# Kernel tuning notes

Measured on AMD Instinct MI355X. Metric: run time of the kernel, lower is better.

The kernel has to match this reference:

```python
import jax, jax.numpy as jnp
import numpy as np

EPS = 1e-9


def _pairwise_sqdist(x1, x2):
    # x1: (B,n,3), x2: (B,m,3) -> (B,n,m) squared euclidean distances
    s1 = jnp.sum(x1 * x1, axis=-1)
    s2 = jnp.sum(x2 * x2, axis=-1)
    cross = jnp.einsum('bnd,bmd->bnm', x1, x2)
    return jnp.maximum(s1[:, :, None] + s2[:, None, :] - 2.0 * cross, 0.0)


def _approxmatch(x1, x2):
    # Faithful port of the approxmatch CUDA kernel (Fan et al. EMD approx).
    B, n, _ = x1.shape
    m = x2.shape[1]
    if n >= m:
        multiL, multiR = 1.0, float(n // m)   # integer division as in CUDA
    else:
        multiL, multiR = float(m // n), 1.0
    dist = _pairwise_sqdist(x1, x2)  # (B,n,m)
    # j = 7 .. -1 -> level = -4^j ; j = -2 -> level = 0  (10 sweeps total)
    levels = jnp.concatenate([
        -(4.0 ** jnp.arange(7, -2, -1, dtype=jnp.float32)),
        jnp.zeros((1,), jnp.float32)])
    match0 = jnp.zeros((B, n, m), jnp.float32)
    remainL0 = jnp.full((B, n), multiL, jnp.float32)
    remainR0 = jnp.full((B, m), multiR, jnp.float32)

    def body(carry, level):
        match, remainL, remainR = carry
        e = jnp.exp(level * dist)                              # (B,n,m)
        suml = EPS + jnp.einsum('bnm,bm->bn', e, remainR)
        ratioL = remainL / suml                                # (B,n)
        sumr = remainR * jnp.einsum('bnm,bn->bm', e, ratioL)   # (B,m)
        consumption = jnp.minimum(remainR / (sumr + EPS), 1.0)
        ratioR = consumption * remainR                         # (B,m)
        remainR = jnp.maximum(0.0, remainR - sumr)
        w = e * ratioL[:, :, None] * ratioR[:, None, :]        # flow k->l
        match = match + w
        remainL = jnp.maximum(0.0, remainL - jnp.sum(w, axis=-1))
        return (match, remainL, remainR), None

    (match, _, _), _ = jax.lax.scan(body, (match0, remainL0, remainR0), levels)
    return match, dist


def setup_inputs() -> dict:
    key = jax.random.key(0)
    k1, k2 = jax.random.split(key)
    B, N = 4, 4096
    xyz1 = jax.random.normal(k1, (B, 3, N), dtype=jnp.float32)
    xyz2 = jax.random.normal(k2, (B, 3, N), dtype=jnp.float32)
    return {"xyz1": xyz1, "xyz2": xyz2}


def reference(xyz1, xyz2):
    # transpose=True: BCN -> BNC
    x1 = jnp.transpose(xyz1, (0, 2, 1))
    x2 = jnp.transpose(xyz2, (0, 2, 1))
    match, dist = _approxmatch(x1, x2)
    d = jnp.sqrt(jnp.maximum(dist, 1e-20))
    cost = jnp.sum(match * d, axis=(1, 2))            # (B,)
    emd = cost / min(x1.shape[1], x2.shape[1])
    return jnp.mean(emd)                               # reduce_mean=True
```

## Files before the change

### kernel.cpp

```cpp
#include <hip/hip_runtime.h>


#define NPTS 4096
#define BATCH 4
#define EMD_EPS 1e-9f
#define TILE 1024
#define RPW 4
#define THREADS 256
#define RPB 16
#define NBLK (NPTS / RPB)
#define NBLK_TOTAL (NBLK * BATCH)

#define GRP_SHIFT 4
#define GRP_SIZE (1 << GRP_SHIFT)
#define NGRP (NBLK_TOTAL / GRP_SIZE)
#define BAR_STRIDE 4352
#define NB_BAR 24

#define CULL_FULL -160.0f
#define CULL_PART -40.0f

typedef float v2f __attribute__((ext_vector_type(2)));

struct Params {
    const float* xyz1;
    const float* xyz2;
    float* remainL;
    float* cost_part;
    float* S_L;
    float* out;
    unsigned* bar;
    float* ratioL[10];
    float* ratioR[9];
    float* remainR[9];
    float ls2[10];
};

struct Smem {
    float4 sA[TILE / 2];
    float4 sB[TILE / 2];
    float2 sC[TILE / 2];
    float  s_cost[THREADS / 64];
};

__device__ __forceinline__ float aload(const float* p_) {
    return __hip_atomic_load((float*)p_, __ATOMIC_RELAXED, __HIP_MEMORY_SCOPE_AGENT);
}
__device__ __forceinline__ void astore(float* p_, float v) {
    __hip_atomic_store(p_, v, __ATOMIC_RELAXED, __HIP_MEMORY_SCOPE_AGENT);
}
__device__ __forceinline__ unsigned au_add(unsigned* p_, unsigned v) {
    return __hip_atomic_fetch_add(p_, v, __ATOMIC_RELAXED, __HIP_MEMORY_SCOPE_AGENT);
}
__device__ __forceinline__ unsigned au_load(const unsigned* p_) {
    return __hip_atomic_load((unsigned*)p_, __ATOMIC_RELAXED, __HIP_MEMORY_SCOPE_AGENT);
}
__device__ __forceinline__ void au_store(unsigned* p_, unsigned v) {
    __hip_atomic_store(p_, v, __ATOMIC_RELAXED, __HIP_MEMORY_SCOPE_AGENT);
}

__device__ __forceinline__ void gsync(unsigned* barbase, int idx) {
    __syncthreads();
    if (threadIdx.x == 0) {
        unsigned* B = barbase + idx * BAR_STRIDE;
        const int bid = blockIdx.y * NBLK + blockIdx.x;
        const int grp = bid >> GRP_SHIFT;
        unsigned* gc   = B + grp * 32;
        unsigned* root = B + NGRP * 32;
        unsigned* gr   = B + NGRP * 32 + 32 + grp * 32;
        unsigned old = au_add(gc, 1u);
        if (old == GRP_SIZE - 1u) {
            unsigned r = au_add(root, 1u) + 1u;
            while (r < (unsigned)NGRP) {
                __builtin_amdgcn_s_sleep(4);
                r = au_load(root);
            }
            au_store(gr, 1u);
        } else {
            while (au_load(gr) == 0u)
                __builtin_amdgcn_s_sleep(4);
        }
        asm volatile("" ::: "memory");
    }
    __syncthreads();
}

__device__ __forceinline__ float fexp2(float x) {
#if __has_builtin(__builtin_amdgcn_exp2f)
    return __builtin_amdgcn_exp2f(x);
#else
    return exp2f(x);
#endif
}
__device__ __forceinline__ float fsqrt(float x) {
#if __has_builtin(__builtin_amdgcn_sqrtf)
    return __builtin_amdgcn_sqrtf(x);
#else
    return __sqrtf(x);
#endif
}

__device__ __forceinline__ float wave_reduce(float v) {
    v += __shfl_xor(v, 32);
    v += __shfl_xor(v, 16);
    v += __shfl_xor(v, 8);
    v += __shfl_xor(v, 4);
    v += __shfl_xor(v, 2);
    v += __shfl_xor(v, 1);
    return v;
}

__device__ __forceinline__ void phase_ratioL0(Smem& sm, const Params& p, float ls2,
                                              float* __restrict__ rLout) {
    const int b = blockIdx.y;
    const int tid = threadIdx.x;
    const int wave = tid >> 6;
    const int lane = tid & 63;
    const int row0 = blockIdx.x * RPB + wave * RPW;

    const float* x1 = p.xyz1 + b * 3 * NPTS;
    const float* x2 = p.xyz2 + b * 3 * NPTS;
    const float2* x2x = (const float2*)(x2);
    const float2* x2y = (const float2*)(x2 + NPTS);
    const float2* x2z = (const float2*)(x2 + 2 * NPTS);

    float px[RPW], py[RPW], pz[RPW];
    v2f acc[RPW];
#pragma unroll
    for (int r = 0; r < RPW; ++r) {
        px[r] = x1[row0 + r];
        py[r] = x1[NPTS + row0 + r];
        pz[r] = x1[2 * NPTS + row0 + r];
        acc[r] = (v2f)(0.0f);
    }
    for (int c0 = 0; c0 < NPTS; c0 += TILE) {
        __syncthreads();
        for (int i = tid; i < TILE / 2; i += THREADS) {
            int e = c0 / 2 + i;
            float2 xx = x2x[e], yy = x2y[e];
            sm.sA[i] = make_float4(xx.x, xx.y, yy.x, yy.y);
            sm.sC[i] = x2z[e];
        }
        __syncthreads();
#pragma unroll 2
        for (int j = 0; j < TILE / 128; ++j) {
            float4 a = sm.sA[lane + 64 * j];
            float2 z = sm.sC[lane + 64 * j];
            v2f ax = {a.x, a.y}, ay = {a.z, a.w}, az = {z.x, z.y};
#pragma unroll
            for (int r = 0; r < RPW; ++r) {
                v2f dx = px[r] - ax, dy = py[r] - ay, dz = pz[r] - az;
                v2f d = dx * dx + dy * dy + dz * dz;
                v2f sd = ls2 * d;
                if (!__all(fmaxf(sd.x, sd.y) < CULL_FULL)) {
                    v2f e2 = {fexp2(sd.x), fexp2(sd.y)};
                    acc[r] += e2;
                }
            }
        }
    }
#pragma unroll
    for (int r = 0; r < RPW; ++r) {
        float s = wave_reduce(acc[r].x + acc[r].y);
        if (lane == 0) {
            int idx = b * NPTS + row0 + r;
            astore(&rLout[idx], 1.0f / (EMD_EPS + s));
            p.remainL[idx] = 1.0f;
        }
    }
}

template <bool CULL>
__device__ __forceinline__ void phase_ratioR(Smem& sm, const Params& p, float ls2,
                                             const float* __restrict__ rL,
                                             const float* __restrict__ rRprev,
                                             float* __restrict__ rRout,
                                             float* __restrict__ remROut) {
    const int b = blockIdx.y;
    const int tid = threadIdx.x;
    const int wave = tid >> 6;
    const int lane = tid & 63;
    const int col0 = blockIdx.x * RPB + wave * RPW;

    const float* x1 = p.xyz1 + b * 3 * NPTS;
    const float* x2 = p.xyz2 + b * 3 * NPTS;
    const float2* x1x = (const float2*)(x1);
    const float2* x1y = (const float2*)(x1 + NPTS);
    const float2* x1z = (const float2*)(x1 + 2 * NPTS);
    const float2* wLv = (const float2*)(rL + b * NPTS);

    float px[RPW], py[RPW], pz[RPW];
    v2f acc[RPW];
#pragma unroll
    for (int r = 0; r < RPW; ++r) {
        px[r] = x2[col0 + r];
        py[r] = x2[NPTS + col0 + r];
        pz[r] = x2[2 * NPTS + col0 + r];
        acc[r] = (v2f)(0.0f);
    }
    for (int c0 = 0; c0 < NPTS; c0 += TILE) {
        __syncthreads();
        for (int i = tid; i < TILE / 2; i += THREADS) {
            int e = c0 / 2 + i;
            float2 xx = x1x[e], yy = x1y[e], zz = x1z[e], ww = wLv[e];
            sm.sA[i] = make_float4(xx.x, xx.y, yy.x, yy.y);
            sm.sB[i] = make_float4(zz.x, zz.y, ww.x, ww.y);
        }
        __syncthreads();
#pragma unroll 2
        for (int j = 0; j < TILE / 128; ++j) {
            float4 a = sm.sA[lane + 64 * j];
            float4 bq = sm.sB[lane + 64 * j];
            v2f ax = {a.x, a.y}, ay = {a.z, a.w};
            v2f az = {bq.x, bq.y}, aw = {bq.z, bq.w};
#pragma unroll
            for (int r = 0; r < RPW; ++r) {
                v2f dx = px[r] - ax, dy = py[r] - ay, dz = pz[r] - az;
                v2f d = dx * dx + dy * dy + dz * dz;
                v2f sd = ls2 * d;
                bool live = true;
                if (CULL) live = !__all(fmaxf(sd.x, sd.y) < CULL_FULL);
                if (live) {
                    v2f e2 = {fexp2(sd.x), fexp2(sd.y)};
                    acc[r] += e2 * aw;
                }
            }
        }
    }
#pragma unroll
    for (int r = 0; r < RPW; ++r) {
        float s = wave_reduce(acc[r].x + acc[r].y);
        if (lane == 0) {
            int idx = b * NPTS + col0 + r;
            float rv = rRprev ? rRprev[idx] : 1.0f;
            float sumr = rv * s;
            float cons = fminf(rv / (sumr + EMD_EPS), 1.0f);
            astore(&rRout[idx], cons * rv);
            astore(&remROut[idx], fmaxf(0.0f, rv - sumr));
        }
    }
}

template <bool SQ, bool CULL>
__device__ __forceinline__ void phase_cost(Smem& sm, const Params& p,
                                           float ls2, float ls2n,
                                           const float* __restrict__ rR,
                                           const float* __restrict__ w2,
                                           const float* __restrict__ rLin,
                                           float* __restrict__ rLout,
                                           int initCost) {
    const int b = blockIdx.y;
    const int tid = threadIdx.x;
    const int wave = tid >> 6;
    const int lane = tid & 63;
    const int row0 = blockIdx.x * RPB + wave * RPW;

    const float* x1 = p.xyz1 + b * 3 * NPTS;
    const float* x2 = p.xyz2 + b * 3 * NPTS;
    const float2* x2x = (const float2*)(x2);
    const float2* x2y = (const float2*)(x2 + NPTS);
    const float2* x2z = (const float2*)(x2 + 2 * NPTS);
    const float2* wRv = (const float2*)(rR + b * NPTS);
    const float2* w2v = (const float2*)(w2 + b * NPTS);

    float px[RPW], py[RPW], pz[RPW];
    v2f acc_a[RPW], acc_c[RPW], acc_s[RPW];
#pragma unroll
    for (int r = 0; r < RPW; ++r) {
        px[r] = x1[row0 + r];
        py[r] = x1[NPTS + row0 + r];
        pz[r] = x1[2 * NPTS + row0 + r];
        acc_a[r] = (v2f)(0.0f);
        acc_c[r] = (v2f)(0.0f);
        acc_s[r] = (v2f)(0.0f);
    }
    for (int c0 = 0; c0 < NPTS; c0 += TILE) {
        __syncthreads();
        for (int i = tid; i < TILE / 2; i += THREADS) {
            int e = c0 / 2 + i;
            float2 xx = x2x[e], yy = x2y[e], zz = x2z[e];
            float2 wr = wRv[e];
            float2 cw = w2v[e];
            sm.sA[i] = make_float4(xx.x, xx.y, yy.x, yy.y);
            sm.sB[i] = make_float4(zz.x, zz.y, wr.x, wr.y);
            sm.sC[i] = cw;
        }
        __syncthreads();
#pragma unroll 2
        for (int j = 0; j < TILE / 128; ++j) {
            float4 a = sm.sA[lane + 64 * j];
            float4 bq = sm.sB[lane + 64 * j];
            float2 c = sm.sC[lane + 64 * j];
            v2f ax = {a.x, a.y}, ay = {a.z, a.w};
            v2f az = {bq.x, bq.y}, wr = {bq.z, bq.w};
            v2f cw = {c.x, c.y};
#pragma unroll
            for (int r = 0; r < RPW; ++r) {
                v2f dx = px[r] - ax, dy = py[r] - ay, dz = pz[r] - az;
                v2f d = dx * dx + dy * dy + dz * dz;
                if (SQ) {
                    v2f sd = ls2n * d;
                    bool fullskip = false, partskip = false;
                    if (CULL) {
                        float mx = fmaxf(sd.x, sd.y);
                        fullskip = __all(mx < CULL_FULL);
                        partskip = __all(mx < CULL_PART);
                    }
                    if (!fullskip) {
                        v2f e2 = {fexp2(sd.x), fexp2(sd.y)};
                        acc_s[r] += e2 * cw;
                        if (!partskip) {
                            v2f e4 = e2 * e2;
                            v2f er = (e4 * e4) * wr;
                            acc_a[r] += er;
                            v2f sq = {fsqrt(d.x), fsqrt(d.y)};
                            acc_c[r] += er * sq;
                        }
                    }
                } else {
                    v2f sd = ls2 * d;
                    v2f e1 = {fexp2(sd.x), fexp2(sd.y)};
                    v2f er = e1 * wr;
                    acc_s[r] += cw;
                    acc_a[r] += er;
                    v2f sq = {fsqrt(d.x), fsqrt(d.y)};
                    acc_c[r] += er * sq;
                }
            }
        }
    }
    float wcost = 0.0f;
#pragma unroll
    for (int r = 0; r < RPW; ++r) {
        float sa = wave_reduce(acc_a[r].x + acc_a[r].y);
        float sc = wave_reduce(acc_c[r].x + acc_c[r].y);
        float ss = wave_reduce(acc_s[r].x + acc_s[r].y);
        if (lane == 0) {
            int idx = b * NPTS + row0 + r;
            float rl = rLin[idx];
            float rem = fmaxf(0.0f, p.remainL[idx] - rl * sa);
            p.remainL[idx] = rem;
            astore(&rLout[idx], rem / (EMD_EPS + ss));
            wcost = fmaf(rl, sc, wcost);
        }
    }
    if (lane == 0) sm.s_cost[wave] = wcost;
    __syncthreads();
    if (tid == 0) {
        float t = sm.s_cost[0] + sm.s_cost[1] + sm.s_cost[2] + sm.s_cost[3];
        int ci = b * NBLK + blockIdx.x;
        astore(&p.cost_part[ci], initCost ? t : aload(&p.cost_part[ci]) + t);
    }
}

__device__ __forceinline__ void phase_sum_ratioL(Smem& sm, const Params& p,
                                                 const float* __restrict__ rL) {
    if (blockIdx.x != 0) return;
    const int b = blockIdx.y;
    const int tid = threadIdx.x;
    float s = 0.0f;
    for (int i = tid; i < NPTS; i += 256) s += rL[b * NPTS + i];
    s = wave_reduce(s);
    if ((tid & 63) == 0) sm.s_cost[tid >> 6] = s;
    __syncthreads();
    if (tid == 0)
        astore(&p.S_L[b], sm.s_cost[0] + sm.s_cost[1] + sm.s_cost[2] + sm.s_cost[3]);
}

__device__ __forceinline__ void phase_cost_l0(Smem& sm, const Params& p,
                                              const float* __restrict__ w2,
                                              const float* __restrict__ rL) {
    const int b = blockIdx.y;
    const int tid = threadIdx.x;
    const int wave = tid >> 6;
    const int lane = tid & 63;
    const int row0 = blockIdx.x * RPB + wave * RPW;
    const float sL = aload(&p.S_L[b]);

    const float* x1 = p.xyz1 + b * 3 * NPTS;
    const float* x2 = p.xyz2 + b * 3 * NPTS;
    const float2* x2x = (const float2*)(x2);
    const float2* x2y = (const float2*)(x2 + NPTS);
    const float2* x2z = (const float2*)(x2 + 2 * NPTS);
    const float2* wRv = (const float2*)(w2 + b * NPTS);

    float px[RPW], py[RPW], pz[RPW];
    v2f acc_c[RPW];
#pragma unroll
    for (int r = 0; r < RPW; ++r) {
        px[r] = x1[row0 + r];
        py[r] = x1[NPTS + row0 + r];
        pz[r] = x1[2 * NPTS + row0 + r];
        acc_c[r] = (v2f)(0.0f);
    }
    for (int c0 = 0; c0 < NPTS; c0 += TILE) {
        __syncthreads();
        for (int i = tid; i < TILE / 2; i += THREADS) {
            int e = c0 / 2 + i;
            float2 xx = x2x[e], yy = x2y[e], zz = x2z[e], rv = wRv[e];
            float wr0 = fminf(rv.x / (rv.x * sL + EMD_EPS), 1.0f) * rv.x;
            float wr1 = fminf(rv.y / (rv.y * sL + EMD_EPS), 1.0f) * rv.y;
            sm.sA[i] = make_float4(xx.x, xx.y, yy.x, yy.y);
            sm.sB[i] = make_float4(zz.x, zz.y, wr0, wr1);
        }
        __syncthreads();
#pragma unroll 2
        for (int j = 0; j < TILE / 128; ++j) {
            float4 a = sm.sA[lane + 64 * j];
            float4 bq = sm.sB[lane + 64 * j];
            v2f ax = {a.x, a.y}, ay = {a.z, a.w};
            v2f az = {bq.x, bq.y}, wr = {bq.z, bq.w};
#pragma unroll
            for (int r = 0; r < RPW; ++r) {
                v2f dx = px[r] - ax, dy = py[r] - ay, dz = pz[r] - az;
                v2f d = dx * dx + dy * dy + dz * dz;
                v2f sq = {fsqrt(d.x), fsqrt(d.y)};
                acc_c[r] += wr * sq;
            }
        }
    }
    float wcost = 0.0f;
#pragma unroll
    for (int r = 0; r < RPW; ++r) {
        float sc = wave_reduce(acc_c[r].x + acc_c[r].y);
        if (lane == 0)
            wcost = fmaf(rL[b * NPTS + row0 + r], sc, wcost);
    }
    if (lane == 0) sm.s_cost[wave] = wcost;
    __syncthreads();
    if (tid == 0) {
        float t = sm.s_cost[0] + sm.s_cost[1] + sm.s_cost[2] + sm.s_cost[3];
        int ci = b * NBLK + blockIdx.x;
        astore(&p.cost_part[ci], aload(&p.cost_part[ci]) + t);
    }
}

__device__ __forceinline__ void phase_final(Smem& sm, const Params& p) {
    if (blockIdx.x != 0 || blockIdx.y != 0) return;
    const int tid = threadIdx.x;
    float s = 0.0f;
    for (int i = tid; i < BATCH * NBLK; i += 256) s += aload(&p.cost_part[i]);
    s = wave_reduce(s);
    if ((tid & 63) == 0) sm.s_cost[tid >> 6] = s;
    __syncthreads();
    if (tid == 0)
        p.out[0] = (sm.s_cost[0] + sm.s_cost[1] + sm.s_cost[2] + sm.s_cost[3]) /
                   ((float)NPTS * (float)BATCH);
}

__global__ __launch_bounds__(THREADS, 4) void k_emd_all(Params p) {
    __shared__ Smem sm;
    int bi = 0;
    phase_ratioL0(sm, p, p.ls2[0], p.ratioL[0]);
    gsync(p.bar, bi++);
    for (int t = 0; t < 9; ++t) {
        const float* rRprev = (t == 0) ? nullptr : p.remainR[t - 1];
        if (t < 4)
            phase_ratioR<true>(sm, p, p.ls2[t], p.ratioL[t], rRprev,
                               p.ratioR[t], p.remainR[t]);
        else
            phase_ratioR<false>(sm, p, p.ls2[t], p.ratioL[t], rRprev,
                                p.ratioR[t], p.remainR[t]);
        gsync(p.bar, bi++);
        if (t < 4)
            phase_cost<true, true>(sm, p, p.ls2[t], p.ls2[t + 1], p.ratioR[t],
                                   p.remainR[t], p.ratioL[t], p.ratioL[t + 1], t == 0);
        else if (t < 8)
            phase_cost<true, false>(sm, p, p.ls2[t], p.ls2[t + 1], p.ratioR[t],
                                    p.remainR[t], p.ratioL[t], p.ratioL[t + 1], 0);
        else
            phase_cost<false, false>(sm, p, p.ls2[8], 0.0f, p.ratioR[8],
                                     p.remainR[8], p.ratioL[8], p.ratioL[9], 0);
        gsync(p.bar, bi++);
    }
    phase_sum_ratioL(sm, p, p.ratioL[9]);
    gsync(p.bar, bi++);
    phase_cost_l0(sm, p, p.remainR[8], p.ratioL[9]);
    gsync(p.bar, bi++);
    phase_final(sm, p);
}

__global__ void k_zero(unsigned* bar) {
    const int n = NB_BAR * BAR_STRIDE;
    for (int i = blockIdx.x * 256 + threadIdx.x; i < n; i += gridDim.x * 256)
        __hip_atomic_store(&bar[i], 0u, __ATOMIC_RELAXED, __HIP_MEMORY_SCOPE_AGENT);
}

__global__ __launch_bounds__(THREADS, 4) void kw_ratioL0(Params p) {
    __shared__ Smem sm;
    phase_ratioL0(sm, p, p.ls2[0], p.ratioL[0]);
}
__global__ __launch_bounds__(THREADS, 4) void kw_ratioR(Params p, int t) {
    __shared__ Smem sm;
    const float* rRprev = (t == 0) ? nullptr : p.remainR[t - 1];
    if (t < 4) phase_ratioR<true>(sm, p, p.ls2[t], p.ratioL[t], rRprev,
                                  p.ratioR[t], p.remainR[t]);
    else       phase_ratioR<false>(sm, p, p.ls2[t], p.ratioL[t], rRprev,
                                   p.ratioR[t], p.remainR[t]);
}
__global__ __launch_bounds__(THREADS, 4) void kw_cost(Params p, int t) {
    __shared__ Smem sm;
    if (t < 4)
        phase_cost<true, true>(sm, p, p.ls2[t], p.ls2[t + 1], p.ratioR[t],
                               p.remainR[t], p.ratioL[t], p.ratioL[t + 1], t == 0);
    else if (t < 8)
        phase_cost<true, false>(sm, p, p.ls2[t], p.ls2[t + 1], p.ratioR[t],
                                p.remainR[t], p.ratioL[t], p.ratioL[t + 1], 0);
    else
        phase_cost<false, false>(sm, p, p.ls2[8], 0.0f, p.ratioR[8],
                                 p.remainR[8], p.ratioL[8], p.ratioL[9], 0);
}
__global__ __launch_bounds__(THREADS, 4) void kw_sum(Params p) {
    __shared__ Smem sm;
    phase_sum_ratioL(sm, p, p.ratioL[9]);
}
__global__ __launch_bounds__(THREADS, 4) void kw_cost_l0(Params p) {
    __shared__ Smem sm;
    phase_cost_l0(sm, p, p.remainR[8], p.ratioL[9]);
}
__global__ __launch_bounds__(THREADS, 4) void kw_final(Params p) {
    __shared__ Smem sm;
    phase_final(sm, p);
}

extern "C" void kernel_launch(void* const* d_in, const int* in_sizes, int n_in,
                              void* d_out, int out_size, void* d_ws, size_t ws_size,
                              hipStream_t stream) {
    Params p;
    p.xyz1 = (const float*)d_in[0];
    p.xyz2 = (const float*)d_in[1];
    const int BN = BATCH * NPTS;
    const int BUF = BN + 1024;
    float* ws = (float*)d_ws;
    p.remainL   = ws;
    p.cost_part = ws + BN;
    p.S_L       = p.cost_part + 2048;
    p.bar       = (unsigned*)(p.S_L + 256);
    float* vbase = (float*)(p.bar + NB_BAR * BAR_STRIDE) + 256;
    for (int t = 0; t < 10; ++t) p.ratioL[t]  = vbase + t * BUF;
    for (int t = 0; t < 9; ++t)  p.ratioR[t]  = vbase + (10 + t) * BUF;
    for (int t = 0; t < 9; ++t)  p.remainR[t] = vbase + (19 + t) * BUF;
    p.out = (float*)d_out;

    static const double levels[10] = {
        -16384.0, -4096.0, -1024.0, -256.0, -64.0,
        -16.0, -4.0, -1.0, -0.25, 0.0};
    for (int t = 0; t < 10; ++t)
        p.ls2[t] = (float)(levels[t] * 1.4426950408889634);

    dim3 grid(NBLK, BATCH), blk(THREADS);

    static int coop_ok = -1;
    if (coop_ok < 0) {
        int v = 0;
        hipDeviceGetAttribute(&v, hipDeviceAttributeCooperativeLaunch, 0);
        coop_ok = v;
    }

    hipError_t err = hipErrorUnknown;
    if (coop_ok) {
        k_zero<<<64, 256, 0, stream>>>(p.bar);
        void* args[] = {(void*)&p};
        err = hipLaunchCooperativeKernel((void*)k_emd_all, grid, blk, args, 0, stream);
    }
    if (err != hipSuccess) {
        kw_ratioL0<<<grid, blk, 0, stream>>>(p);
        for (int t = 0; t < 9; ++t) {
            kw_ratioR<<<grid, blk, 0, stream>>>(p, t);
            kw_cost<<<grid, blk, 0, stream>>>(p, t);
        }
        kw_sum<<<dim3(1, BATCH), blk, 0, stream>>>(p);
        kw_cost_l0<<<grid, blk, 0, stream>>>(p);
        kw_final<<<dim3(1, 1), blk, 0, stream>>>(p);
    }
}
```

Measured before the change: 655.7 us.

## Stage full point clouds in LDS once and use 1024-thread blocks

```diff
diff --git a/kernel.cpp b/kernel.cpp
--- a/kernel.cpp
+++ b/kernel.cpp
@@ -4,12 +4,13 @@
 #define NPTS 4096
 #define BATCH 4
 #define EMD_EPS 1e-9f
-#define TILE 1024
 #define RPW 4
-#define THREADS 256
-#define RPB 16
+#define THREADS 1024
+#define NWAVE (THREADS / 64)
+#define RPB (NWAVE * RPW)
 #define NBLK (NPTS / RPB)
 #define NBLK_TOTAL (NBLK * BATCH)
+#define NJ (NPTS / 128)
 
 #define GRP_SHIFT 4
 #define GRP_SIZE (1 << GRP_SHIFT)
@@ -37,10 +38,15 @@
 };
 
 struct Smem {
-    float4 sA[TILE / 2];
-    float4 sB[TILE / 2];
-    float2 sC[TILE / 2];
-    float  s_cost[THREADS / 64];
+    alignas(16) float x1x[NPTS];
+    alignas(16) float x1y[NPTS];
+    alignas(16) float x1z[NPTS];
+    alignas(16) float x2x[NPTS];
+    alignas(16) float x2y[NPTS];
+    alignas(16) float x2z[NPTS];
+    alignas(16) float sW[NPTS];
+    alignas(16) float sV[NPTS];
+    float s_cost[NWAVE];
 };
 
 __device__ __forceinline__ float aload(const float* p_) {
@@ -110,6 +116,30 @@
     return v;
 }
 
+__device__ __forceinline__ void stage_xyz(Smem& sm, const Params& p) {
+    const int b = blockIdx.y;
+    const int i = threadIdx.x;
+    const float4* g1 = (const float4*)(p.xyz1 + b * 3 * NPTS);
+    const float4* g2 = (const float4*)(p.xyz2 + b * 3 * NPTS);
+    ((float4*)sm.x1x)[i] = g1[i];
+    ((float4*)sm.x1y)[i] = g1[NPTS / 4 + i];
+    ((float4*)sm.x1z)[i] = g1[2 * (NPTS / 4) + i];
+    ((float4*)sm.x2x)[i] = g2[i];
+    ((float4*)sm.x2y)[i] = g2[NPTS / 4 + i];
+    ((float4*)sm.x2z)[i] = g2[2 * (NPTS / 4) + i];
+    __syncthreads();
+}
+
+__device__ __forceinline__ void stage_w1(Smem& sm, const float* gw) {
+    ((float4*)sm.sW)[threadIdx.x] = ((const float4*)gw)[threadIdx.x];
+    __syncthreads();
+}
+__device__ __forceinline__ void stage_w2(Smem& sm, const float* gw, const float* gv) {
+    ((float4*)sm.sW)[threadIdx.x] = ((const float4*)gw)[threadIdx.x];
+    ((float4*)sm.sV)[threadIdx.x] = ((const float4*)gv)[threadIdx.x];
+    __syncthreads();
+}
+
 __device__ __forceinline__ void phase_ratioL0(Smem& sm, const Params& p, float ls2,
                                               float* __restrict__ rLout) {
     const int b = blockIdx.y;
@@ -118,44 +148,30 @@
     const int lane = tid & 63;
     const int row0 = blockIdx.x * RPB + wave * RPW;
 
-    const float* x1 = p.xyz1 + b * 3 * NPTS;
-    const float* x2 = p.xyz2 + b * 3 * NPTS;
-    const float2* x2x = (const float2*)(x2);
-    const float2* x2y = (const float2*)(x2 + NPTS);
-    const float2* x2z = (const float2*)(x2 + 2 * NPTS);
-
     float px[RPW], py[RPW], pz[RPW];
     v2f acc[RPW];
 #pragma unroll
     for (int r = 0; r < RPW; ++r) {
-        px[r] = x1[row0 + r];
-        py[r] = x1[NPTS + row0 + r];
-        pz[r] = x1[2 * NPTS + row0 + r];
+        px[r] = sm.x1x[row0 + r];
+        py[r] = sm.x1y[row0 + r];
+        pz[r] = sm.x1z[row0 + r];
         acc[r] = (v2f)(0.0f);
     }
-    for (int c0 = 0; c0 < NPTS; c0 += TILE) {
-        __syncthreads();
-        for (int i = tid; i < TILE / 2; i += THREADS) {
-            int e = c0 / 2 + i;
-            float2 xx = x2x[e], yy = x2y[e];
-            sm.sA[i] = make_float4(xx.x, xx.y, yy.x, yy.y);
-            sm.sC[i] = x2z[e];
-        }
-        __syncthreads();
+    const v2f* vx = (const v2f*)sm.x2x;
+    const v2f* vy = (const v2f*)sm.x2y;
+    const v2f* vz = (const v2f*)sm.x2z;
 #pragma unroll 2
-        for (int j = 0; j < TILE / 128; ++j) {
-            float4 a = sm.sA[lane + 64 * j];
-            float2 z = sm.sC[lane + 64 * j];
-            v2f ax = {a.x, a.y}, ay = {a.z, a.w}, az = {z.x, z.y};
-#pragma unroll
-            for (int r = 0; r < RPW; ++r) {
-                v2f dx = px[r] - ax, dy = py[r] - ay, dz = pz[r] - az;
-                v2f d = dx * dx + dy * dy + dz * dz;
-                v2f sd = ls2 * d;
-                if (!__all(fmaxf(sd.x, sd.y) < CULL_FULL)) {
-                    v2f e2 = {fexp2(sd.x), fexp2(sd.y)};
-                    acc[r] += e2;
-                }
+    for (int j = 0; j < NJ; ++j) {
+        int cp = lane + 64 * j;
+        v2f ax = vx[cp], ay = vy[cp], az = vz[cp];
+#pragma unroll
+        for (int r = 0; r < RPW; ++r) {
+            v2f dx = px[r] - ax, dy = py[r] - ay, dz = pz[r] - az;
+            v2f d = dx * dx + dy * dy + dz * dz;
+            v2f sd = ls2 * d;
+            if (!__all(fmaxf(sd.x, sd.y) < CULL_FULL)) {
+                v2f e2 = {fexp2(sd.x), fexp2(sd.y)};
+                acc[r] += e2;
             }
         }
     }
@@ -182,48 +198,35 @@
     const int lane = tid & 63;
     const int col0 = blockIdx.x * RPB + wave * RPW;
 
-    const float* x1 = p.xyz1 + b * 3 * NPTS;
-    const float* x2 = p.xyz2 + b * 3 * NPTS;
-    const float2* x1x = (const float2*)(x1);
-    const float2* x1y = (const float2*)(x1 + NPTS);
-    const float2* x1z = (const float2*)(x1 + 2 * NPTS);
-    const float2* wLv = (const float2*)(rL + b * NPTS);
+    stage_w1(sm, rL + b * NPTS);
 
     float px[RPW], py[RPW], pz[RPW];
     v2f acc[RPW];
 #pragma unroll
     for (int r = 0; r < RPW; ++r) {
-        px[r] = x2[col0 + r];
-        py[r] = x2[NPTS + col0 + r];
-        pz[r] = x2[2 * NPTS + col0 + r];
+        px[r] = sm.x2x[col0 + r];
+        py[r] = sm.x2y[col0 + r];
+        pz[r] = sm.x2z[col0 + r];
         acc[r] = (v2f)(0.0f);
     }
-    for (int c0 = 0; c0 < NPTS; c0 += TILE) {
-        __syncthreads();
-        for (int i = tid; i < TILE / 2; i += THREADS) {
-            int e = c0 / 2 + i;
-            float2 xx = x1x[e], yy = x1y[e], zz = x1z[e], ww = wLv[e];
-            sm.sA[i] = make_float4(xx.x, xx.y, yy.x, yy.y);
-            sm.sB[i] = make_float4(zz.x, zz.y, ww.x, ww.y);
-        }
-        __syncthreads();
+    const v2f* vx = (const v2f*)sm.x1x;
+    const v2f* vy = (const v2f*)sm.x1y;
+    const v2f* vz = (const v2f*)sm.x1z;
+    const v2f* vw = (const v2f*)sm.sW;
 #pragma unroll 2
-        for (int j = 0; j < TILE / 128; ++j) {
-            float4 a = sm.sA[lane + 64 * j];
-            float4 bq = sm.sB[lane + 64 * j];
-            v2f ax = {a.x, a.y}, ay = {a.z, a.w};
-            v2f az = {bq.x, bq.y}, aw = {bq.z, bq.w};
-#pragma unroll
-            for (int r = 0; r < RPW; ++r) {
-                v2f dx = px[r] - ax, dy = py[r] - ay, dz = pz[r] - az;
-                v2f d = dx * dx + dy * dy + dz * dz;
-                v2f sd = ls2 * d;
-                bool live = true;
-                if (CULL) live = !__all(fmaxf(sd.x, sd.y) < CULL_FULL);
-                if (live) {
-                    v2f e2 = {fexp2(sd.x), fexp2(sd.y)};
-                    acc[r] += e2 * aw;
-                }
+    for (int j = 0; j < NJ; ++j) {
+        int cp = lane + 64 * j;
+        v2f ax = vx[cp], ay = vy[cp], az = vz[cp], aw = vw[cp];
+#pragma unroll
+        for (int r = 0; r < RPW; ++r) {
+            v2f dx = px[r] - ax, dy = py[r] - ay, dz = pz[r] - az;
+            v2f d = dx * dx + dy * dy + dz * dz;
+            v2f sd = ls2 * d;
+            bool live = true;
+            if (CULL) live = !__all(fmaxf(sd.x, sd.y) < CULL_FULL);
+            if (live) {
+                v2f e2 = {fexp2(sd.x), fexp2(sd.y)};
+                acc[r] += e2 * aw;
             }
         }
     }
@@ -255,77 +258,60 @@
     const int lane = tid & 63;
     const int row0 = blockIdx.x * RPB + wave * RPW;
 
-    const float* x1 = p.xyz1 + b * 3 * NPTS;
-    const float* x2 = p.xyz2 + b * 3 * NPTS;
-    const float2* x2x = (const float2*)(x2);
-    const float2* x2y = (const float2*)(x2 + NPTS);
-    const float2* x2z = (const float2*)(x2 + 2 * NPTS);
-    const float2* wRv = (const float2*)(rR + b * NPTS);
-    const float2* w2v = (const float2*)(w2 + b * NPTS);
+    stage_w2(sm, rR + b * NPTS, w2 + b * NPTS);
 
     float px[RPW], py[RPW], pz[RPW];
     v2f acc_a[RPW], acc_c[RPW], acc_s[RPW];
 #pragma unroll
     for (int r = 0; r < RPW; ++r) {
-        px[r] = x1[row0 + r];
-        py[r] = x1[NPTS + row0 + r];
-        pz[r] = x1[2 * NPTS + row0 + r];
+        px[r] = sm.x1x[row0 + r];
+        py[r] = sm.x1y[row0 + r];
+        pz[r] = sm.x1z[row0 + r];
         acc_a[r] = (v2f)(0.0f);
         acc_c[r] = (v2f)(0.0f);
         acc_s[r] = (v2f)(0.0f);
     }
-    for (int c0 = 0; c0 < NPTS; c0 += TILE) {
-        __syncthreads();
-        for (int i = tid; i < TILE / 2; i += THREADS) {
-            int e = c0 / 2 + i;
-            float2 xx = x2x[e], yy = x2y[e], zz = x2z[e];
-            float2 wr = wRv[e];
-            float2 cw = w2v[e];
-            sm.sA[i] = make_float4(xx.x, xx.y, yy.x, yy.y);
-            sm.sB[i] = make_float4(zz.x, zz.y, wr.x, wr.y);
-            sm.sC[i] = cw;
-        }
-        __syncthreads();
+    const v2f* vx = (const v2f*)sm.x2x;
+    const v2f* vy = (const v2f*)sm.x2y;
+    const v2f* vz = (const v2f*)sm.x2z;
+    const v2f* vw = (const v2f*)sm.sW;
+    const v2f* vv = (const v2f*)sm.sV;
 #pragma unroll 2
-        for (int j = 0; j < TILE / 128; ++j) {
-            float4 a = sm.sA[lane + 64 * j];
-            float4 bq = sm.sB[lane + 64 * j];
-            float2 c = sm.sC[lane + 64 * j];
-            v2f ax = {a.x, a.y}, ay = {a.z, a.w};
-            v2f az = {bq.x, bq.y}, wr = {bq.z, bq.w};
-            v2f cw = {c.x, c.y};
-#pragma unroll
-            for (int r = 0; r < RPW; ++r) {
-                v2f dx = px[r] - ax, dy = py[r] - ay, dz = pz[r] - az;
-                v2f d = dx * dx + dy * dy + dz * dz;
-                if (SQ) {
-                    v2f sd = ls2n * d;
-                    bool fullskip = false, partskip = false;
-                    if (CULL) {
-                        float mx = fmaxf(sd.x, sd.y);
-                        fullskip = __all(mx < CULL_FULL);
-                        partskip = __all(mx < CULL_PART);
+    for (int j = 0; j < NJ; ++j) {
+        int cp = lane + 64 * j;
+        v2f ax = vx[cp], ay = vy[cp], az = vz[cp];
+        v2f wr = vw[cp], cw = vv[cp];
+#pragma unroll
+        for (int r = 0; r < RPW; ++r) {
+            v2f dx = px[r] - ax, dy = py[r] - ay, dz = pz[r] - az;
+            v2f d = dx * dx + dy * dy + dz * dz;
+            if (SQ) {
+                v2f sd = ls2n * d;
+                bool fullskip = false, partskip = false;
+                if (CULL) {
+                    float mx = fmaxf(sd.x, sd.y);
+                    fullskip = __all(mx < CULL_FULL);
+                    partskip = __all(mx < CULL_PART);
+                }
+                if (!fullskip) {
+                    v2f e2 = {fexp2(sd.x), fexp2(sd.y)};
+                    acc_s[r] += e2 * cw;
+                    if (!partskip) {
+                        v2f e4 = e2 * e2;
+                        v2f er = (e4 * e4) * wr;
+                        acc_a[r] += er;
+                        v2f sq = {fsqrt(d.x), fsqrt(d.y)};
+                        acc_c[r] += er * sq;
                     }
-                    if (!fullskip) {
-                        v2f e2 = {fexp2(sd.x), fexp2(sd.y)};
-                        acc_s[r] += e2 * cw;
-                        if (!partskip) {
-                            v2f e4 = e2 * e2;
-                            v2f er = (e4 * e4) * wr;
-                            acc_a[r] += er;
-                            v2f sq = {fsqrt(d.x), fsqrt(d.y)};
-                            acc_c[r] += er * sq;
-                        }
-                    }
-                } else {
-                    v2f sd = ls2 * d;
-                    v2f e1 = {fexp2(sd.x), fexp2(sd.y)};
-                    v2f er = e1 * wr;
-                    acc_s[r] += cw;
-                    acc_a[r] += er;
-                    v2f sq = {fsqrt(d.x), fsqrt(d.y)};
-                    acc_c[r] += er * sq;
                 }
+            } else {
+                v2f sd = ls2 * d;
+                v2f e1 = {fexp2(sd.x), fexp2(sd.y)};
+                v2f er = e1 * wr;
+                acc_s[r] += cw;
+                acc_a[r] += er;
+                v2f sq = {fsqrt(d.x), fsqrt(d.y)};
+                acc_c[r] += er * sq;
             }
         }
     }
@@ -347,7 +333,8 @@
     if (lane == 0) sm.s_cost[wave] = wcost;
     __syncthreads();
     if (tid == 0) {
-        float t = sm.s_cost[0] + sm.s_cost[1] + sm.s_cost[2] + sm.s_cost[3];
+        float t = 0.0f;
+        for (int w = 0; w < NWAVE; ++w) t += sm.s_cost[w];
         int ci = b * NBLK + blockIdx.x;
         astore(&p.cost_part[ci], initCost ? t : aload(&p.cost_part[ci]) + t);
     }
@@ -359,12 +346,15 @@
     const int b = blockIdx.y;
     const int tid = threadIdx.x;
     float s = 0.0f;
-    for (int i = tid; i < NPTS; i += 256) s += rL[b * NPTS + i];
+    for (int i = tid; i < NPTS; i += THREADS) s += rL[b * NPTS + i];
     s = wave_reduce(s);
     if ((tid & 63) == 0) sm.s_cost[tid >> 6] = s;
     __syncthreads();
-    if (tid == 0)
-        astore(&p.S_L[b], sm.s_cost[0] + sm.s_cost[1] + sm.s_cost[2] + sm.s_cost[3]);
+    if (tid == 0) {
+        float t = 0.0f;
+        for (int w = 0; w < NWAVE; ++w) t += sm.s_cost[w];
+        astore(&p.S_L[b], t);
+    }
 }
 
 __device__ __forceinline__ void phase_cost_l0(Smem& sm, const Params& p,
@@ -377,46 +367,40 @@
     const int row0 = blockIdx.x * RPB + wave * RPW;
     const float sL = aload(&p.S_L[b]);
 
-    const float* x1 = p.xyz1 + b * 3 * NPTS;
-    const float* x2 = p.xyz2 + b * 3 * NPTS;
-    const float2* x2x = (const float2*)(x2);
-    const float2* x2y = (const float2*)(x2 + NPTS);
-    const float2* x2z = (const float2*)(x2 + 2 * NPTS);
-    const float2* wRv = (const float2*)(w2 + b * NPTS);
+    {
+        float4 rv = ((const float4*)(w2 + b * NPTS))[tid];
+        float4 w;
+        w.x = fminf(rv.x / (rv.x * sL + EMD_EPS), 1.0f) * rv.x;
+        w.y = fminf(rv.y / (rv.y * sL + EMD_EPS), 1.0f) * rv.y;
+        w.z = fminf(rv.z / (rv.z * sL + EMD_EPS), 1.0f) * rv.z;
+        w.w = fminf(rv.w / (rv.w * sL + EMD_EPS), 1.0f) * rv.w;
+        ((float4*)sm.sW)[tid] = w;
+        __syncthreads();
+    }
 
     float px[RPW], py[RPW], pz[RPW];
     v2f acc_c[RPW];
 #pragma unroll
     for (int r = 0; r < RPW; ++r) {
-        px[r] = x1[row0 + r];
-        py[r] = x1[NPTS + row0 + r];
-        pz[r] = x1[2 * NPTS + row0 + r];
+        px[r] = sm.x1x[row0 + r];
+        py[r] = sm.x1y[row0 + r];
+        pz[r] = sm.x1z[row0 + r];
         acc_c[r] = (v2f)(0.0f);
     }
-    for (int c0 = 0; c0 < NPTS; c0 += TILE) {
-        __syncthreads();
-        for (int i = tid; i < TILE / 2; i += THREADS) {
-            int e = c0 / 2 + i;
-            float2 xx = x2x[e], yy = x2y[e], zz = x2z[e], rv = wRv[e];
-            float wr0 = fminf(rv.x / (rv.x * sL + EMD_EPS), 1.0f) * rv.x;
-            float wr1 = fminf(rv.y / (rv.y * sL + EMD_EPS), 1.0f) * rv.y;
-            sm.sA[i] = make_float4(xx.x, xx.y, yy.x, yy.y);
-            sm.sB[i] = make_float4(zz.x, zz.y, wr0, wr1);
-        }
-        __syncthreads();
+    const v2f* vx = (const v2f*)sm.x2x;
+    const v2f* vy = (const v2f*)sm.x2y;
+    const v2f* vz = (const v2f*)sm.x2z;
+    const v2f* vw = (const v2f*)sm.sW;
 #pragma unroll 2
-        for (int j = 0; j < TILE / 128; ++j) {
-            float4 a = sm.sA[lane + 64 * j];
-            float4 bq = sm.sB[lane + 64 * j];
-            v2f ax = {a.x, a.y}, ay = {a.z, a.w};
-            v2f az = {bq.x, bq.y}, wr = {bq.z, bq.w};
-#pragma unroll
-            for (int r = 0; r < RPW; ++r) {
-                v2f dx = px[r] - ax, dy = py[r] - ay, dz = pz[r] - az;
-                v2f d = dx * dx + dy * dy + dz * dz;
-                v2f sq = {fsqrt(d.x), fsqrt(d.y)};
-                acc_c[r] += wr * sq;
-            }
+    for (int j = 0; j < NJ; ++j) {
+        int cp = lane + 64 * j;
+        v2f ax = vx[cp], ay = vy[cp], az = vz[cp], wr = vw[cp];
+#pragma unroll
+        for (int r = 0; r < RPW; ++r) {
+            v2f dx = px[r] - ax, dy = py[r] - ay, dz = pz[r] - az;
+            v2f d = dx * dx + dy * dy + dz * dz;
+            v2f sq = {fsqrt(d.x), fsqrt(d.y)};
+            acc_c[r] += wr * sq;
         }
     }
     float wcost = 0.0f;
@@ -429,7 +413,8 @@
     if (lane == 0) sm.s_cost[wave] = wcost;
     __syncthreads();
     if (tid == 0) {
-        float t = sm.s_cost[0] + sm.s_cost[1] + sm.s_cost[2] + sm.s_cost[3];
+        float t = 0.0f;
+        for (int w = 0; w < NWAVE; ++w) t += sm.s_cost[w];
         int ci = b * NBLK + blockIdx.x;
         astore(&p.cost_part[ci], aload(&p.cost_part[ci]) + t);
     }
@@ -439,17 +424,20 @@
     if (blockIdx.x != 0 || blockIdx.y != 0) return;
     const int tid = threadIdx.x;
     float s = 0.0f;
-    for (int i = tid; i < BATCH * NBLK; i += 256) s += aload(&p.cost_part[i]);
+    for (int i = tid; i < BATCH * NBLK; i += THREADS) s += aload(&p.cost_part[i]);
     s = wave_reduce(s);
     if ((tid & 63) == 0) sm.s_cost[tid >> 6] = s;
     __syncthreads();
-    if (tid == 0)
-        p.out[0] = (sm.s_cost[0] + sm.s_cost[1] + sm.s_cost[2] + sm.s_cost[3]) /
-                   ((float)NPTS * (float)BATCH);
+    if (tid == 0) {
+        float t = 0.0f;
+        for (int w = 0; w < NWAVE; ++w) t += sm.s_cost[w];
+        p.out[0] = t / ((float)NPTS * (float)BATCH);
+    }
 }
 
 __global__ __launch_bounds__(THREADS, 4) void k_emd_all(Params p) {
     __shared__ Smem sm;
+    stage_xyz(sm, p);
     int bi = 0;
     phase_ratioL0(sm, p, p.ls2[0], p.ratioL[0]);
     gsync(p.bar, bi++);
@@ -488,10 +476,12 @@
 
 __global__ __launch_bounds__(THREADS, 4) void kw_ratioL0(Params p) {
     __shared__ Smem sm;
+    stage_xyz(sm, p);
     phase_ratioL0(sm, p, p.ls2[0], p.ratioL[0]);
 }
 __global__ __launch_bounds__(THREADS, 4) void kw_ratioR(Params p, int t) {
     __shared__ Smem sm;
+    stage_xyz(sm, p);
     const float* rRprev = (t == 0) ? nullptr : p.remainR[t - 1];
     if (t < 4) phase_ratioR<true>(sm, p, p.ls2[t], p.ratioL[t], rRprev,
                                   p.ratioR[t], p.remainR[t]);
@@ -500,6 +490,7 @@
 }
 __global__ __launch_bounds__(THREADS, 4) void kw_cost(Params p, int t) {
     __shared__ Smem sm;
+    stage_xyz(sm, p);
     if (t < 4)
         phase_cost<true, true>(sm, p, p.ls2[t], p.ls2[t + 1], p.ratioR[t],
                                p.remainR[t], p.ratioL[t], p.ratioL[t + 1], t == 0);
@@ -516,6 +507,7 @@
 }
 __global__ __launch_bounds__(THREADS, 4) void kw_cost_l0(Params p) {
     __shared__ Smem sm;
+    stage_xyz(sm, p);
     phase_cost_l0(sm, p, p.remainR[8], p.ratioL[9]);
 }
 __global__ __launch_bounds__(THREADS, 4) void kw_final(Params p) {
```

Result: faster. 533.0 us (-18.7%).
